# Optimization experiments

Measured on AMD Instinct MI355X. Metric: run time of the kernel, lower is better.

Reference implementation:

```python
import jax, jax.numpy as jnp
import numpy as np

D_MODEL = 1024
DIM_FF = 4096
N_EXPERTS = 8
TOPK = 2
N_TOKENS = 8192


def setup_inputs() -> dict:
    key = jax.random.key(0)
    ks = jax.random.split(key, 8)
    s_in = 1.0 / np.sqrt(D_MODEL)
    s_ff = 1.0 / np.sqrt(DIM_FF)
    x = jax.random.normal(ks[0], (N_TOKENS, D_MODEL), dtype=jnp.float32)
    Wg = jax.random.uniform(ks[1], (D_MODEL, N_EXPERTS), minval=-s_in, maxval=s_in, dtype=jnp.float32)
    bg = jax.random.uniform(ks[2], (N_EXPERTS,), minval=-s_in, maxval=s_in, dtype=jnp.float32)
    W1 = jax.random.uniform(ks[3], (N_EXPERTS, D_MODEL, DIM_FF), minval=-s_in, maxval=s_in, dtype=jnp.float32)
    b1 = jax.random.uniform(ks[4], (N_EXPERTS, DIM_FF), minval=-s_in, maxval=s_in, dtype=jnp.float32)
    W2 = jax.random.uniform(ks[5], (N_EXPERTS, DIM_FF, D_MODEL), minval=-s_ff, maxval=s_ff, dtype=jnp.float32)
    b2 = jax.random.uniform(ks[6], (N_EXPERTS, D_MODEL), minval=-s_ff, maxval=s_ff, dtype=jnp.float32)
    return {"x": x, "Wg": Wg, "bg": bg, "W1": W1, "b1": b1, "W2": W2, "b2": b2}


def reference(x, Wg, bg, W1, b1, W2, b2):
    # Gate: softmax over experts
    w = jax.nn.softmax(x @ Wg + bg, axis=-1)  # [N, E]
    # Sparse gating: keep top-k, renormalize (matches torch scatter mask)
    _, idx = jax.lax.top_k(w, TOPK)  # [N, K]
    n = w.shape[0]
    mask = jnp.zeros_like(w).at[jnp.arange(n)[:, None], idx].set(1.0)
    w = w * mask
    w = w / (jnp.sum(w, axis=-1, keepdims=True) + 1e-9)
    # Dense per-expert FFN (exact GELU, as torch nn.GELU default)
    h = jax.nn.gelu(jnp.einsum('nd,edf->enf', x, W1) + b1[:, None, :], approximate=False)  # [E,N,F]
    y = jnp.einsum('enf,efd->end', h, W2) + b2[:, None, :]  # [E,N,D]
    out = jnp.einsum('ne,end->nd', w, y)  # weighted combine
    return out
```

## Files before the change

kernel.cpp:

```cpp
#include <hip/hip_runtime.h>
#include <cstdint>

typedef unsigned short u16;
typedef unsigned int u32;

#define N_TOKENS 8192
#define D_MODEL 1024
#define DIM_FF 4096
#define N_EXPERTS 8
#define MAX_SLOTS (N_TOKENS * 2)

typedef __bf16 bf16x8 __attribute__((ext_vector_type(8)));
typedef float f32x4 __attribute__((ext_vector_type(4)));

__device__ __forceinline__ u16 f2bf(float f) {
  u32 u = __float_as_uint(f);
  u32 r = (u + 0x7FFFu + ((u >> 16) & 1u)) >> 16;
  return (u16)r;
}

__device__ __forceinline__ void gl2lds16(const void* g, void* l) {
  __builtin_amdgcn_global_load_lds(
      (__attribute__((address_space(1))) void*)(g),
      (__attribute__((address_space(3))) void*)(l), 16, 0, 0);
}

__global__ __launch_bounds__(256) void gate_kernel(
    const float* __restrict__ x, const float* __restrict__ Wg,
    const float* __restrict__ bg, int* __restrict__ eidx,
    float* __restrict__ ew) {
  int tok = (int)((blockIdx.x * 256 + threadIdx.x) >> 6);
  int lane = threadIdx.x & 63;
  const float* xr = x + (size_t)tok * D_MODEL;
  float acc[8] = {0.f, 0.f, 0.f, 0.f, 0.f, 0.f, 0.f, 0.f};
  for (int j = 0; j < 16; ++j) {
    int d = lane + 64 * j;
    float xv = xr[d];
    float4 wa = *(const float4*)(Wg + d * 8);
    float4 wb = *(const float4*)(Wg + d * 8 + 4);
    acc[0] += xv * wa.x; acc[1] += xv * wa.y; acc[2] += xv * wa.z; acc[3] += xv * wa.w;
    acc[4] += xv * wb.x; acc[5] += xv * wb.y; acc[6] += xv * wb.z; acc[7] += xv * wb.w;
  }
#pragma unroll
  for (int off = 32; off > 0; off >>= 1) {
#pragma unroll
    for (int e = 0; e < 8; ++e) acc[e] += __shfl_xor(acc[e], off, 64);
  }
  if (lane == 0) {
    float p[8], m = -1e30f;
#pragma unroll
    for (int e = 0; e < 8; ++e) { p[e] = acc[e] + bg[e]; m = fmaxf(m, p[e]); }
    float s = 0.f;
#pragma unroll
    for (int e = 0; e < 8; ++e) { p[e] = __expf(p[e] - m); s += p[e]; }
#pragma unroll
    for (int e = 0; e < 8; ++e) p[e] /= s;
    int i0 = 0;
#pragma unroll
    for (int e = 1; e < 8; ++e) if (p[e] > p[i0]) i0 = e;
    int i1 = (i0 == 0) ? 1 : 0;
#pragma unroll
    for (int e = 0; e < 8; ++e) if (e != i0 && p[e] > p[i1]) i1 = e;
    float denom = p[i0] + p[i1] + 1e-9f;
    eidx[2 * tok] = i0; eidx[2 * tok + 1] = i1;
    ew[2 * tok] = p[i0] / denom; ew[2 * tok + 1] = p[i1] / denom;
  }
}

__global__ __launch_bounds__(256) void count_kernel(const int* __restrict__ eidx,
                                                    int* __restrict__ counts) {
  __shared__ int lc[N_EXPERTS];
  int tid = threadIdx.x;
  if (tid < N_EXPERTS) lc[tid] = 0;
  __syncthreads();
  int t = blockIdx.x * 256 + tid;
  atomicAdd(&lc[eidx[2 * t]], 1);
  atomicAdd(&lc[eidx[2 * t + 1]], 1);
  __syncthreads();
  if (tid < N_EXPERTS) atomicAdd(&counts[tid], lc[tid]);
}

__global__ void scan_kernel(const int* __restrict__ counts, int* __restrict__ offsets) {
  if (threadIdx.x == 0) {
    int o = 0;
    for (int e = 0; e < N_EXPERTS; ++e) { offsets[e] = o; o += counts[e]; }
    offsets[N_EXPERTS] = o;
  }
}

__global__ __launch_bounds__(256) void fill_kernel(
    const int* __restrict__ eidx, const float* __restrict__ ew,
    const int* __restrict__ offsets, int* __restrict__ fill,
    int* __restrict__ rowtok, float* __restrict__ rowwt,
    int* __restrict__ tokslot) {
  __shared__ int lc[N_EXPERTS];
  __shared__ int lbase[N_EXPERTS];
  int tid = threadIdx.x;
  if (tid < N_EXPERTS) lc[tid] = 0;
  __syncthreads();
  int t = blockIdx.x * 256 + tid;
  int e0 = eidx[2 * t], e1 = eidx[2 * t + 1];
  int p0 = atomicAdd(&lc[e0], 1);
  int p1 = atomicAdd(&lc[e1], 1);
  __syncthreads();
  if (tid < N_EXPERTS) lbase[tid] = atomicAdd(&fill[tid], lc[tid]);
  __syncthreads();
  int pos0 = offsets[e0] + lbase[e0] + p0;
  int pos1 = offsets[e1] + lbase[e1] + p1;
  rowtok[pos0] = t; rowwt[pos0] = ew[2 * t];     tokslot[2 * t] = pos0;
  rowtok[pos1] = t; rowwt[pos1] = ew[2 * t + 1]; tokslot[2 * t + 1] = pos1;
}

__global__ __launch_bounds__(256) void cvt_x_kernel(const float* __restrict__ in,
                                                    u16* __restrict__ out) {
  size_t t = (size_t)blockIdx.x * 256 + threadIdx.x;
  const float4* ip = (const float4*)in + t * 2;
  float4 a = ip[0], b = ip[1];
  uint4 o;
  o.x = f2bf(a.x) | ((u32)f2bf(a.y) << 16);
  o.y = f2bf(a.z) | ((u32)f2bf(a.w) << 16);
  o.z = f2bf(b.x) | ((u32)f2bf(b.y) << 16);
  o.w = f2bf(b.z) | ((u32)f2bf(b.w) << 16);
  *((uint4*)out + t) = o;
}

__global__ __launch_bounds__(256) void transpose_cvt(const float* __restrict__ in,
                                                     u16* __restrict__ out, int R, int C) {
  int e = blockIdx.z;
  const float* ip = in + (size_t)e * R * C;
  u16* op = out + (size_t)e * R * C;
  int r0 = blockIdx.y * 64, c0 = blockIdx.x * 64;
  __shared__ __align__(16) u16 t[64 * 72];
  int tid = threadIdx.x;
  int i = tid >> 4;
  int j4 = (tid & 15) * 4;
  for (int p = 0; p < 4; ++p, i += 16) {
    float4 v = *(const float4*)(ip + (size_t)(r0 + i) * C + c0 + j4);
    t[(j4 + 0) * 72 + i] = f2bf(v.x);
    t[(j4 + 1) * 72 + i] = f2bf(v.y);
    t[(j4 + 2) * 72 + i] = f2bf(v.z);
    t[(j4 + 3) * 72 + i] = f2bf(v.w);
  }
  __syncthreads();
#pragma unroll
  for (int p = 0; p < 2; ++p) {
    int c = p * 256 + tid;
    int j = c >> 3, i0 = (c & 7) * 8;
    uint4 val = *(const uint4*)&t[j * 72 + i0];
    *(uint4*)(op + (size_t)(c0 + j) * R + r0 + i0) = val;
  }
}

__global__ __launch_bounds__(256) void fc1_kernel(
    const u16* __restrict__ xb, const u16* __restrict__ w1t,
    const float* __restrict__ b1, const int* __restrict__ rowtok,
    const int* __restrict__ offsets, u16* __restrict__ H) {
  const int b = blockIdx.x;
  const int e = b & 7;
  const int lin = b >> 3;
  const int rt = lin & 63;
  const int ct = lin >> 6;
  const int base = offsets[e];
  const int count = offsets[e + 1] - base;
  if (rt * 128 >= count) return;

  __shared__ __align__(16) __bf16 As[128 * 32];
  __shared__ __align__(16) __bf16 Bs[128 * 32];

  const int tid = threadIdx.x;
  const int lane = tid & 63;
  const int wave = tid >> 6;

  const int ra = tid >> 2;
  const int lastslot = base + count - 1;
  int s0 = base + rt * 128 + ra;       if (s0 > lastslot) s0 = lastslot;
  int s1 = base + rt * 128 + ra + 64;  if (s1 > lastslot) s1 = lastslot;
  const size_t koff = (size_t)(tid & 3) * 8;
  const u16* ga0 = xb + (size_t)rowtok[s0] * D_MODEL + koff;
  const u16* ga1 = xb + (size_t)rowtok[s1] * D_MODEL + koff;
  const u16* gb0 = w1t + (size_t)e * DIM_FF * D_MODEL + (size_t)(ct * 128 + ra) * D_MODEL + koff;
  const u16* gb1 = gb0 + (size_t)64 * D_MODEL;

  __bf16* lA0 = As + tid * 8;
  __bf16* lA1 = As + (tid + 256) * 8;
  __bf16* lB0 = Bs + tid * 8;
  __bf16* lB1 = Bs + (tid + 256) * 8;

  const int wm = (wave & 1) * 64;
  const int wn = (wave >> 1) * 64;
  const int quad = lane >> 4;
  const int lc = lane & 15;
  const __bf16* Ap = As + (wm + lc) * 32 + quad * 8;
  const __bf16* Bp = Bs + (wn + lc) * 32 + quad * 8;

  f32x4 acc[4][4];
#pragma unroll
  for (int i = 0; i < 4; ++i)
#pragma unroll
    for (int j = 0; j < 4; ++j) acc[i][j] = (f32x4)0.0f;

  for (int kt = 0; kt < D_MODEL / 32; ++kt) {
    gl2lds16(ga0 + kt * 32, lA0);
    gl2lds16(ga1 + kt * 32, lA1);
    gl2lds16(gb0 + kt * 32, lB0);
    gl2lds16(gb1 + kt * 32, lB1);
    __syncthreads();
    bf16x8 af[4], bfr[4];
#pragma unroll
    for (int mi = 0; mi < 4; ++mi) af[mi] = *(const bf16x8*)(Ap + mi * 16 * 32);
#pragma unroll
    for (int ni = 0; ni < 4; ++ni) bfr[ni] = *(const bf16x8*)(Bp + ni * 16 * 32);
#pragma unroll
    for (int mi = 0; mi < 4; ++mi)
#pragma unroll
      for (int ni = 0; ni < 4; ++ni)
        acc[mi][ni] = __builtin_amdgcn_mfma_f32_16x16x32_bf16(af[mi], bfr[ni], acc[mi][ni], 0, 0, 0);
    __syncthreads();
  }

  float bias[4];
#pragma unroll
  for (int ni = 0; ni < 4; ++ni) bias[ni] = b1[e * DIM_FF + ct * 128 + wn + ni * 16 + lc];
#pragma unroll
  for (int mi = 0; mi < 4; ++mi) {
#pragma unroll
    for (int r = 0; r < 4; ++r) {
      int m = wm + mi * 16 + quad * 4 + r;
      int grow = rt * 128 + m;
      if (grow < count) {
        size_t rowbase = (size_t)(base + grow) * DIM_FF + ct * 128 + wn;
#pragma unroll
        for (int ni = 0; ni < 4; ++ni) {
          float v = acc[mi][ni][r] + bias[ni];
          float t3 = v * (1.0f + 0.044715f * v * v);
          float u = __builtin_amdgcn_exp2f(fminf(2.302208f * t3, 80.0f));
          float h = v * u * __builtin_amdgcn_rcpf(u + 1.0f);
          H[rowbase + ni * 16 + lc] = f2bf(h);
        }
      }
    }
  }
}

__global__ __launch_bounds__(256) void fc2_kernel(
    const u16* __restrict__ H, const u16* __restrict__ w2t,
    const float* __restrict__ b2, const int* __restrict__ rowtok,
    const float* __restrict__ rowwt, const int* __restrict__ offsets,
    float* __restrict__ y, float* __restrict__ out, int use_y) {
  const int b = blockIdx.x;
  const int e = b & 7;
  const int lin = b >> 3;
  const int rt = lin & 63;
  const int ct = lin >> 6;
  const int base = offsets[e];
  const int count = offsets[e + 1] - base;
  if (rt * 128 >= count) return;

  __shared__ __align__(16) __bf16 As[128 * 32];
  __shared__ __align__(16) __bf16 Bs[128 * 32];

  const int tid = threadIdx.x;
  const int lane = tid & 63;
  const int wave = tid >> 6;

  const int ra = tid >> 2;
  const size_t koff = (size_t)(tid & 3) * 8;
  const u16* ga0 = H + (size_t)(base + rt * 128 + ra) * DIM_FF + koff;
  const u16* ga1 = ga0 + (size_t)64 * DIM_FF;
  const u16* gb0 = w2t + (size_t)e * D_MODEL * DIM_FF + (size_t)(ct * 128 + ra) * DIM_FF + koff;
  const u16* gb1 = gb0 + (size_t)64 * DIM_FF;

  __bf16* lA0 = As + tid * 8;
  __bf16* lA1 = As + (tid + 256) * 8;
  __bf16* lB0 = Bs + tid * 8;
  __bf16* lB1 = Bs + (tid + 256) * 8;

  const int wm = (wave & 1) * 64;
  const int wn = (wave >> 1) * 64;
  const int quad = lane >> 4;
  const int lc = lane & 15;
  const __bf16* Ap = As + (wm + lc) * 32 + quad * 8;
  const __bf16* Bp = Bs + (wn + lc) * 32 + quad * 8;

  f32x4 acc[4][4];
#pragma unroll
  for (int i = 0; i < 4; ++i)
#pragma unroll
    for (int j = 0; j < 4; ++j) acc[i][j] = (f32x4)0.0f;

  for (int kt = 0; kt < DIM_FF / 32; ++kt) {
    gl2lds16(ga0 + kt * 32, lA0);
    gl2lds16(ga1 + kt * 32, lA1);
    gl2lds16(gb0 + kt * 32, lB0);
    gl2lds16(gb1 + kt * 32, lB1);
    __syncthreads();
    bf16x8 af[4], bfr[4];
#pragma unroll
    for (int mi = 0; mi < 4; ++mi) af[mi] = *(const bf16x8*)(Ap + mi * 16 * 32);
#pragma unroll
    for (int ni = 0; ni < 4; ++ni) bfr[ni] = *(const bf16x8*)(Bp + ni * 16 * 32);
#pragma unroll
    for (int mi = 0; mi < 4; ++mi)
#pragma unroll
      for (int ni = 0; ni < 4; ++ni)
        acc[mi][ni] = __builtin_amdgcn_mfma_f32_16x16x32_bf16(af[mi], bfr[ni], acc[mi][ni], 0, 0, 0);
    __syncthreads();
  }

  float bias[4];
#pragma unroll
  for (int ni = 0; ni < 4; ++ni) bias[ni] = b2[e * D_MODEL + ct * 128 + wn + ni * 16 + lc];

  if (use_y) {
#pragma unroll
    for (int mi = 0; mi < 4; ++mi) {
#pragma unroll
      for (int r = 0; r < 4; ++r) {
        int m = wm + mi * 16 + quad * 4 + r;
        int grow = rt * 128 + m;
        if (grow < count) {
          float* yrow = y + (size_t)(base + grow) * D_MODEL + ct * 128 + wn;
#pragma unroll
          for (int ni = 0; ni < 4; ++ni) yrow[ni * 16 + lc] = acc[mi][ni][r] + bias[ni];
        }
      }
    }
  } else {
#pragma unroll
    for (int mi = 0; mi < 4; ++mi) {
#pragma unroll
      for (int r = 0; r < 4; ++r) {
        int m = wm + mi * 16 + quad * 4 + r;
        int grow = rt * 128 + m;
        if (grow < count) {
          int slot = base + grow;
          float wt = rowwt[slot];
          float* orow = out + (size_t)rowtok[slot] * D_MODEL + ct * 128 + wn;
#pragma unroll
          for (int ni = 0; ni < 4; ++ni)
            atomicAdd(orow + ni * 16 + lc, wt * (acc[mi][ni][r] + bias[ni]));
        }
      }
    }
  }
}

__global__ __launch_bounds__(256) void combine_kernel(
    const float* __restrict__ y, const int* __restrict__ tokslot,
    const float* __restrict__ ew, float* __restrict__ out) {
  int gid = blockIdx.x * 256 + threadIdx.x;
  int t = gid >> 8;
  int c = (gid & 255) * 4;
  int s0 = tokslot[2 * t], s1 = tokslot[2 * t + 1];
  float w0 = ew[2 * t], w1 = ew[2 * t + 1];
  float4 a = *(const float4*)(y + (size_t)s0 * D_MODEL + c);
  float4 bb = *(const float4*)(y + (size_t)s1 * D_MODEL + c);
  float4 o;
  o.x = w0 * a.x + w1 * bb.x;
  o.y = w0 * a.y + w1 * bb.y;
  o.z = w0 * a.z + w1 * bb.z;
  o.w = w0 * a.w + w1 * bb.w;
  *(float4*)(out + (size_t)t * D_MODEL + c) = o;
}

extern "C" void kernel_launch(void* const* d_in, const int* in_sizes, int n_in,
                              void* d_out, int out_size, void* d_ws, size_t ws_size,
                              hipStream_t stream) {
  (void)in_sizes; (void)n_in;
  const float* x  = (const float*)d_in[0];
  const float* Wg = (const float*)d_in[1];
  const float* bg = (const float*)d_in[2];
  const float* W1 = (const float*)d_in[3];
  const float* b1 = (const float*)d_in[4];
  const float* W2 = (const float*)d_in[5];
  const float* b2 = (const float*)d_in[6];
  float* out = (float*)d_out;

  char* ws = (char*)d_ws;
  size_t off = 0;
  int*   counts  = (int*)(ws + 0);
  int*   fill    = (int*)(ws + 64);
  int*   offsets = (int*)(ws + 128);
  off = 4096;
  int*   eidx    = (int*)(ws + off); off += 65536;
  float* ew      = (float*)(ws + off); off += 65536;
  int*   rowtok  = (int*)(ws + off); off += 65536;
  float* rowwt   = (float*)(ws + off); off += 65536;
  int*   tokslot = (int*)(ws + off); off += 65536;
  u16*   xb      = (u16*)(ws + off); off += (size_t)N_TOKENS * D_MODEL * 2;
  u16*   w1t     = (u16*)(ws + off);
  u16*   w2t     = w1t;
  off += (size_t)N_EXPERTS * DIM_FF * D_MODEL * 2;
  u16*   H       = (u16*)(ws + off);
  off += (size_t)(MAX_SLOTS + 128) * DIM_FF * 2;
  float* y       = (float*)(ws + off);
  size_t need_y  = off + (size_t)MAX_SLOTS * D_MODEL * 4;
  const int use_y = (ws_size >= need_y) ? 1 : 0;

  hipMemsetAsync(ws, 0, 4096, stream);
  if (!use_y) hipMemsetAsync(d_out, 0, (size_t)out_size * sizeof(float), stream);

  gate_kernel<<<N_TOKENS / 4, 256, 0, stream>>>(x, Wg, bg, eidx, ew);
  count_kernel<<<N_TOKENS / 256, 256, 0, stream>>>(eidx, counts);
  scan_kernel<<<1, 64, 0, stream>>>(counts, offsets);
  fill_kernel<<<N_TOKENS / 256, 256, 0, stream>>>(eidx, ew, offsets, fill, rowtok, rowwt, tokslot);
  cvt_x_kernel<<<(N_TOKENS * D_MODEL / 8) / 256, 256, 0, stream>>>(x, xb);
  transpose_cvt<<<dim3(DIM_FF / 64, D_MODEL / 64, N_EXPERTS), 256, 0, stream>>>(W1, w1t, D_MODEL, DIM_FF);
  fc1_kernel<<<N_EXPERTS * (DIM_FF / 128) * 64, 256, 0, stream>>>(xb, w1t, b1, rowtok, offsets, H);
  transpose_cvt<<<dim3(D_MODEL / 64, DIM_FF / 64, N_EXPERTS), 256, 0, stream>>>(W2, w2t, DIM_FF, D_MODEL);
  fc2_kernel<<<N_EXPERTS * (D_MODEL / 128) * 64, 256, 0, stream>>>(H, w2t, b2, rowtok, rowwt, offsets, y, out, use_y);
  if (use_y)
    combine_kernel<<<(N_TOKENS * D_MODEL / 4) / 256, 256, 0, stream>>>(y, tokslot, ew, out);
}
```

Baseline: 782.4 us.

## Split routing slots by top-k rank and combine directly in two fc2 passes

Slots are now grouped by (expert, top-k rank), giving 16 segments. fc2 runs twice: the first pass writes the weighted result straight into the output, and the second adds into it without atomics, since each token appears at most once per rank. This removes the fp32 y intermediate (about 64 MB written and read back) and the separate combine kernel. The transpose tile also grows to 128 rows. The cost is a second fc2 launch that serialises the ranks, with possibly lower occupancy per pass, plus read-modify-write traffic on the output.

```diff
diff --git a/kernel.cpp b/kernel.cpp
--- a/kernel.cpp
+++ b/kernel.cpp
@@ -69,46 +69,45 @@
 
 __global__ __launch_bounds__(256) void count_kernel(const int* __restrict__ eidx,
                                                     int* __restrict__ counts) {
-  __shared__ int lc[N_EXPERTS];
+  __shared__ int lc[16];
   int tid = threadIdx.x;
-  if (tid < N_EXPERTS) lc[tid] = 0;
+  if (tid < 16) lc[tid] = 0;
   __syncthreads();
   int t = blockIdx.x * 256 + tid;
-  atomicAdd(&lc[eidx[2 * t]], 1);
-  atomicAdd(&lc[eidx[2 * t + 1]], 1);
-  __syncthreads();
-  if (tid < N_EXPERTS) atomicAdd(&counts[tid], lc[tid]);
-}
-
-__global__ void scan_kernel(const int* __restrict__ counts, int* __restrict__ offsets) {
+  atomicAdd(&lc[2 * eidx[2 * t]], 1);
+  atomicAdd(&lc[2 * eidx[2 * t + 1] + 1], 1);
+  __syncthreads();
+  if (tid < 16) atomicAdd(&counts[tid], lc[tid]);
+}
+
+__global__ void scan_kernel(const int* __restrict__ counts, int* __restrict__ off16) {
   if (threadIdx.x == 0) {
     int o = 0;
-    for (int e = 0; e < N_EXPERTS; ++e) { offsets[e] = o; o += counts[e]; }
-    offsets[N_EXPERTS] = o;
+    for (int g = 0; g < 16; ++g) { off16[g] = o; o += counts[g]; }
+    off16[16] = o;
   }
 }
 
 __global__ __launch_bounds__(256) void fill_kernel(
     const int* __restrict__ eidx, const float* __restrict__ ew,
-    const int* __restrict__ offsets, int* __restrict__ fill,
-    int* __restrict__ rowtok, float* __restrict__ rowwt,
-    int* __restrict__ tokslot) {
-  __shared__ int lc[N_EXPERTS];
-  __shared__ int lbase[N_EXPERTS];
+    const int* __restrict__ off16, int* __restrict__ fill,
+    int* __restrict__ rowtok, float* __restrict__ rowwt) {
+  __shared__ int lc[16];
+  __shared__ int lbase[16];
   int tid = threadIdx.x;
-  if (tid < N_EXPERTS) lc[tid] = 0;
+  if (tid < 16) lc[tid] = 0;
   __syncthreads();
   int t = blockIdx.x * 256 + tid;
   int e0 = eidx[2 * t], e1 = eidx[2 * t + 1];
-  int p0 = atomicAdd(&lc[e0], 1);
-  int p1 = atomicAdd(&lc[e1], 1);
-  __syncthreads();
-  if (tid < N_EXPERTS) lbase[tid] = atomicAdd(&fill[tid], lc[tid]);
-  __syncthreads();
-  int pos0 = offsets[e0] + lbase[e0] + p0;
-  int pos1 = offsets[e1] + lbase[e1] + p1;
-  rowtok[pos0] = t; rowwt[pos0] = ew[2 * t];     tokslot[2 * t] = pos0;
-  rowtok[pos1] = t; rowwt[pos1] = ew[2 * t + 1]; tokslot[2 * t + 1] = pos1;
+  int p0 = atomicAdd(&lc[2 * e0], 1);
+  int p1 = atomicAdd(&lc[2 * e1 + 1], 1);
+  __syncthreads();
+  if (tid < 16) lbase[tid] = atomicAdd(&fill[tid], lc[tid]);
+  __syncthreads();
+  int pos0 = off16[2 * e0] + lbase[2 * e0] + p0;
+  int pos1 = off16[2 * e1 + 1] + lbase[2 * e1 + 1] + p1;
+  rowtok[pos0] = t; rowwt[pos0] = ew[2 * t];
+  rowtok[pos1] = t; rowwt[pos1] = ew[2 * t + 1];
 }
 
 __global__ __launch_bounds__(256) void cvt_x_kernel(const float* __restrict__ in,
@@ -129,39 +128,40 @@
   int e = blockIdx.z;
   const float* ip = in + (size_t)e * R * C;
   u16* op = out + (size_t)e * R * C;
-  int r0 = blockIdx.y * 64, c0 = blockIdx.x * 64;
-  __shared__ __align__(16) u16 t[64 * 72];
+  int c0 = blockIdx.x * 64, r0 = blockIdx.y * 128;
+  __shared__ __align__(16) u16 t[64 * 136];
   int tid = threadIdx.x;
-  int i = tid >> 4;
   int j4 = (tid & 15) * 4;
-  for (int p = 0; p < 4; ++p, i += 16) {
+#pragma unroll
+  for (int p = 0; p < 8; ++p) {
+    int i = (tid >> 4) + 16 * p;
     float4 v = *(const float4*)(ip + (size_t)(r0 + i) * C + c0 + j4);
-    t[(j4 + 0) * 72 + i] = f2bf(v.x);
-    t[(j4 + 1) * 72 + i] = f2bf(v.y);
-    t[(j4 + 2) * 72 + i] = f2bf(v.z);
-    t[(j4 + 3) * 72 + i] = f2bf(v.w);
-  }
-  __syncthreads();
-#pragma unroll
-  for (int p = 0; p < 2; ++p) {
-    int c = p * 256 + tid;
-    int j = c >> 3, i0 = (c & 7) * 8;
-    uint4 val = *(const uint4*)&t[j * 72 + i0];
-    *(uint4*)(op + (size_t)(c0 + j) * R + r0 + i0) = val;
+    t[(j4 + 0) * 136 + i] = f2bf(v.x);
+    t[(j4 + 1) * 136 + i] = f2bf(v.y);
+    t[(j4 + 2) * 136 + i] = f2bf(v.z);
+    t[(j4 + 3) * 136 + i] = f2bf(v.w);
+  }
+  __syncthreads();
+  int i8 = (tid & 15) * 8;
+#pragma unroll
+  for (int p = 0; p < 4; ++p) {
+    int c = (tid >> 4) + 16 * p;
+    uint4 val = *(const uint4*)&t[c * 136 + i8];
+    *(uint4*)(op + (size_t)(c0 + c) * R + r0 + i8) = val;
   }
 }
 
 __global__ __launch_bounds__(256) void fc1_kernel(
     const u16* __restrict__ xb, const u16* __restrict__ w1t,
     const float* __restrict__ b1, const int* __restrict__ rowtok,
-    const int* __restrict__ offsets, u16* __restrict__ H) {
+    const int* __restrict__ off16, u16* __restrict__ H) {
   const int b = blockIdx.x;
   const int e = b & 7;
   const int lin = b >> 3;
   const int rt = lin & 63;
   const int ct = lin >> 6;
-  const int base = offsets[e];
-  const int count = offsets[e + 1] - base;
+  const int base = off16[2 * e];
+  const int count = off16[2 * e + 2] - base;
   if (rt * 128 >= count) return;
 
   __shared__ __align__(16) __bf16 As[128 * 32];
@@ -245,16 +245,16 @@
 __global__ __launch_bounds__(256) void fc2_kernel(
     const u16* __restrict__ H, const u16* __restrict__ w2t,
     const float* __restrict__ b2, const int* __restrict__ rowtok,
-    const float* __restrict__ rowwt, const int* __restrict__ offsets,
-    float* __restrict__ y, float* __restrict__ out, int use_y) {
+    const float* __restrict__ rowwt, const int* __restrict__ off16,
+    float* __restrict__ out, int kpass) {
   const int b = blockIdx.x;
   const int e = b & 7;
   const int lin = b >> 3;
   const int rt = lin & 63;
   const int ct = lin >> 6;
-  const int base = offsets[e];
-  const int count = offsets[e + 1] - base;
-  if (rt * 128 >= count) return;
+  const int base = off16[2 * e + kpass];
+  const int cnt  = off16[2 * e + kpass + 1] - base;
+  if (rt * 128 >= cnt) return;
 
   __shared__ __align__(16) __bf16 As[128 * 32];
   __shared__ __align__(16) __bf16 Bs[128 * 32];
@@ -311,62 +311,34 @@
 #pragma unroll
   for (int ni = 0; ni < 4; ++ni) bias[ni] = b2[e * D_MODEL + ct * 128 + wn + ni * 16 + lc];
 
-  if (use_y) {
-#pragma unroll
-    for (int mi = 0; mi < 4; ++mi) {
-#pragma unroll
-      for (int r = 0; r < 4; ++r) {
-        int m = wm + mi * 16 + quad * 4 + r;
-        int grow = rt * 128 + m;
-        if (grow < count) {
-          float* yrow = y + (size_t)(base + grow) * D_MODEL + ct * 128 + wn;
-#pragma unroll
-          for (int ni = 0; ni < 4; ++ni) yrow[ni * 16 + lc] = acc[mi][ni][r] + bias[ni];
+#pragma unroll
+  for (int mi = 0; mi < 4; ++mi) {
+#pragma unroll
+    for (int r = 0; r < 4; ++r) {
+      int m = wm + mi * 16 + quad * 4 + r;
+      int grow = rt * 128 + m;
+      if (grow < cnt) {
+        int slot = base + grow;
+        float wt = rowwt[slot];
+        float* orow = out + (size_t)rowtok[slot] * D_MODEL + ct * 128 + wn;
+        if (kpass == 0) {
+#pragma unroll
+          for (int ni = 0; ni < 4; ++ni)
+            orow[ni * 16 + lc] = wt * (acc[mi][ni][r] + bias[ni]);
+        } else {
+#pragma unroll
+          for (int ni = 0; ni < 4; ++ni)
+            orow[ni * 16 + lc] += wt * (acc[mi][ni][r] + bias[ni]);
         }
       }
     }
-  } else {
-#pragma unroll
-    for (int mi = 0; mi < 4; ++mi) {
-#pragma unroll
-      for (int r = 0; r < 4; ++r) {
-        int m = wm + mi * 16 + quad * 4 + r;
-        int grow = rt * 128 + m;
-        if (grow < count) {
-          int slot = base + grow;
-          float wt = rowwt[slot];
-          float* orow = out + (size_t)rowtok[slot] * D_MODEL + ct * 128 + wn;
-#pragma unroll
-          for (int ni = 0; ni < 4; ++ni)
-            atomicAdd(orow + ni * 16 + lc, wt * (acc[mi][ni][r] + bias[ni]));
-        }
-      }
-    }
-  }
-}
-
-__global__ __launch_bounds__(256) void combine_kernel(
-    const float* __restrict__ y, const int* __restrict__ tokslot,
-    const float* __restrict__ ew, float* __restrict__ out) {
-  int gid = blockIdx.x * 256 + threadIdx.x;
-  int t = gid >> 8;
-  int c = (gid & 255) * 4;
-  int s0 = tokslot[2 * t], s1 = tokslot[2 * t + 1];
-  float w0 = ew[2 * t], w1 = ew[2 * t + 1];
-  float4 a = *(const float4*)(y + (size_t)s0 * D_MODEL + c);
-  float4 bb = *(const float4*)(y + (size_t)s1 * D_MODEL + c);
-  float4 o;
-  o.x = w0 * a.x + w1 * bb.x;
-  o.y = w0 * a.y + w1 * bb.y;
-  o.z = w0 * a.z + w1 * bb.z;
-  o.w = w0 * a.w + w1 * bb.w;
-  *(float4*)(out + (size_t)t * D_MODEL + c) = o;
+  }
 }
 
 extern "C" void kernel_launch(void* const* d_in, const int* in_sizes, int n_in,
                               void* d_out, int out_size, void* d_ws, size_t ws_size,
                               hipStream_t stream) {
-  (void)in_sizes; (void)n_in;
+  (void)in_sizes; (void)n_in; (void)ws_size; (void)out_size;
   const float* x  = (const float*)d_in[0];
   const float* Wg = (const float*)d_in[1];
   const float* bg = (const float*)d_in[2];
@@ -379,36 +351,30 @@
   char* ws = (char*)d_ws;
   size_t off = 0;
   int*   counts  = (int*)(ws + 0);
-  int*   fill    = (int*)(ws + 64);
-  int*   offsets = (int*)(ws + 128);
+  int*   fill    = (int*)(ws + 128);
+  int*   off16   = (int*)(ws + 256);
   off = 4096;
   int*   eidx    = (int*)(ws + off); off += 65536;
   float* ew      = (float*)(ws + off); off += 65536;
   int*   rowtok  = (int*)(ws + off); off += 65536;
   float* rowwt   = (float*)(ws + off); off += 65536;
-  int*   tokslot = (int*)(ws + off); off += 65536;
   u16*   xb      = (u16*)(ws + off); off += (size_t)N_TOKENS * D_MODEL * 2;
   u16*   w1t     = (u16*)(ws + off);
   u16*   w2t     = w1t;
   off += (size_t)N_EXPERTS * DIM_FF * D_MODEL * 2;
   u16*   H       = (u16*)(ws + off);
   off += (size_t)(MAX_SLOTS + 128) * DIM_FF * 2;
-  float* y       = (float*)(ws + off);
-  size_t need_y  = off + (size_t)MAX_SLOTS * D_MODEL * 4;
-  const int use_y = (ws_size >= need_y) ? 1 : 0;
 
   hipMemsetAsync(ws, 0, 4096, stream);
-  if (!use_y) hipMemsetAsync(d_out, 0, (size_t)out_size * sizeof(float), stream);
 
   gate_kernel<<<N_TOKENS / 4, 256, 0, stream>>>(x, Wg, bg, eidx, ew);
   count_kernel<<<N_TOKENS / 256, 256, 0, stream>>>(eidx, counts);
-  scan_kernel<<<1, 64, 0, stream>>>(counts, offsets);
-  fill_kernel<<<N_TOKENS / 256, 256, 0, stream>>>(eidx, ew, offsets, fill, rowtok, rowwt, tokslot);
+  scan_kernel<<<1, 64, 0, stream>>>(counts, off16);
+  fill_kernel<<<N_TOKENS / 256, 256, 0, stream>>>(eidx, ew, off16, fill, rowtok, rowwt);
   cvt_x_kernel<<<(N_TOKENS * D_MODEL / 8) / 256, 256, 0, stream>>>(x, xb);
-  transpose_cvt<<<dim3(DIM_FF / 64, D_MODEL / 64, N_EXPERTS), 256, 0, stream>>>(W1, w1t, D_MODEL, DIM_FF);
-  fc1_kernel<<<N_EXPERTS * (DIM_FF / 128) * 64, 256, 0, stream>>>(xb, w1t, b1, rowtok, offsets, H);
-  transpose_cvt<<<dim3(D_MODEL / 64, DIM_FF / 64, N_EXPERTS), 256, 0, stream>>>(W2, w2t, DIM_FF, D_MODEL);
-  fc2_kernel<<<N_EXPERTS * (D_MODEL / 128) * 64, 256, 0, stream>>>(H, w2t, b2, rowtok, rowwt, offsets, y, out, use_y);
-  if (use_y)
-    combine_kernel<<<(N_TOKENS * D_MODEL / 4) / 256, 256, 0, stream>>>(y, tokslot, ew, out);
-}
+  transpose_cvt<<<dim3(DIM_FF / 64, D_MODEL / 128, N_EXPERTS), 256, 0, stream>>>(W1, w1t, D_MODEL, DIM_FF);
+  fc1_kernel<<<N_EXPERTS * (DIM_FF / 128) * 64, 256, 0, stream>>>(xb, w1t, b1, rowtok, off16, H);
+  transpose_cvt<<<dim3(D_MODEL / 64, DIM_FF / 128, N_EXPERTS), 256, 0, stream>>>(W2, w2t, DIM_FF, D_MODEL);
+  fc2_kernel<<<N_EXPERTS * (D_MODEL / 128) * 64, 256, 0, stream>>>(H, w2t, b2, rowtok, rowwt, off16, out, 0);
+  fc2_kernel<<<N_EXPERTS * (D_MODEL / 128) * 64, 256, 0, stream>>>(H, w2t, b2, rowtok, rowwt, off16, out, 1);
+}
```

Result: no change. 781.5 us (-0.1%).
